# Kernel optimization log

Hardware: AMD Instinct MI355X
Metric: run time of the kernel (lower is better)

Reference implementation:

```python
import jax, jax.numpy as jnp
import numpy as np
import math

C = 512          # channels
K = 3            # conv kernel size
DILATIONS = (1, 3, 5)
RATIO = 2        # up/down sample ratio
FK = 12          # FIR anti-alias kernel size


def kaiser_sinc_filter1d(cutoff, half_width, kernel_size):
    # BigVGAN alias-free kaiser-windowed sinc lowpass filter
    half_size = kernel_size // 2
    delta_f = 4.0 * half_width
    A = 2.285 * (half_size - 1) * math.pi * delta_f + 7.95
    if A > 50.0:
        beta = 0.1102 * (A - 8.7)
    elif A >= 21.0:
        beta = 0.5842 * (A - 21.0) ** 0.4 + 0.07886 * (A - 21.0)
    else:
        beta = 0.0
    window = np.kaiser(kernel_size, beta)
    if kernel_size % 2 == 0:
        time = np.arange(-half_size, half_size) + 0.5
    else:
        time = np.arange(kernel_size) - half_size
    filt = 2.0 * cutoff * window * np.sinc(2.0 * cutoff * time)
    filt = filt / filt.sum()
    return jnp.asarray(filt, dtype=jnp.float32)

# Up/Down both use cutoff=0.5/ratio, half_width=0.6/ratio, kernel=12
AA_FILTER = kaiser_sinc_filter1d(0.5 / RATIO, 0.6 / RATIO, FK)

UP_PAD = FK // RATIO - 1                               # 5 (replicate pad before transpose conv)
UP_PAD_LEFT = UP_PAD * RATIO + (FK - RATIO) // 2       # 15
UP_PAD_RIGHT = UP_PAD * RATIO + (FK - RATIO + 1) // 2  # 15
DN_PAD_LEFT = FK // 2 - 1                              # 5 (even kernel)
DN_PAD_RIGHT = FK // 2                                 # 6


def _depthwise_conv(x, filt, stride=1, lhs_dilation=1, padding=(0, 0)):
    c = x.shape[1]
    w = jnp.broadcast_to(filt.reshape(1, 1, -1), (c, 1, filt.shape[0]))
    return jax.lax.conv_general_dilated(
        x, w, window_strides=(stride,), padding=[padding],
        lhs_dilation=(lhs_dilation,), dimension_numbers=('NCH', 'OIH', 'NCH'),
        feature_group_count=c)


def upsample2x(x):
    # replicate pad, depthwise transposed conv (lhs-dilated conv w/ flipped kernel), crop, scale
    x = jnp.pad(x, ((0, 0), (0, 0), (UP_PAD, UP_PAD)), mode='edge')
    y = RATIO * _depthwise_conv(x, AA_FILTER[::-1], lhs_dilation=RATIO,
                                padding=(FK - 1, FK - 1))
    return y[..., UP_PAD_LEFT:-UP_PAD_RIGHT]


def downsample2x(x):
    x = jnp.pad(x, ((0, 0), (0, 0), (DN_PAD_LEFT, DN_PAD_RIGHT)), mode='edge')
    return _depthwise_conv(x, AA_FILTER, stride=RATIO)


def snake_log(x, alpha, beta):
    # use_log_scale=True: alpha/beta are exponentiated; x + 1/(b+1e-5) * sin(a*x)^2
    a = jnp.exp(alpha)[None, :, None]
    b = jnp.exp(beta)[None, :, None]
    return x + (1.0 / (b + 1e-5)) * jnp.square(jnp.sin(x * a))


def aliasing_activation(x, alpha, beta):
    return downsample2x(snake_log(upsample2x(x), alpha, beta))


def weight_norm_conv1d(x, v, g, bias, dilation):
    # torch weight_norm dim=0: W[o] = g[o] * v[o] / ||v[o]||
    norm = jnp.sqrt(jnp.sum(v * v, axis=(1, 2), keepdims=True))
    w = g[:, None, None] * v / norm
    pad = (K * dilation - dilation) // 2
    y = jax.lax.conv_general_dilated(
        x, w, window_strides=(1,), padding=[(pad, pad)],
        rhs_dilation=(dilation,), dimension_numbers=('NCH', 'OIH', 'NCH'))
    return y + bias[None, :, None]


def setup_inputs() -> dict:
    key = jax.random.key(0)
    ks = jax.random.split(key, 12)
    B, T = 16, 4096
    return {
        'x': jax.random.normal(ks[0], (B, C, T), dtype=jnp.float32),
        'float_masks': jnp.ones((B, 1, T), dtype=jnp.float32),
        'in_snake_alpha': 0.1 * jax.random.normal(ks[1], (3, C), dtype=jnp.float32),
        'in_snake_beta': 0.1 * jax.random.normal(ks[2], (3, C), dtype=jnp.float32),
        'out_snake_alpha': 0.1 * jax.random.normal(ks[3], (3, C), dtype=jnp.float32),
        'out_snake_beta': 0.1 * jax.random.normal(ks[4], (3, C), dtype=jnp.float32),
        'in_conv_v': 0.05 * jax.random.normal(ks[5], (3, C, C, K), dtype=jnp.float32),
        'in_conv_g': 1.0 + 0.01 * jax.random.normal(ks[6], (3, C), dtype=jnp.float32),
        'in_conv_b': 0.01 * jax.random.normal(ks[7], (3, C), dtype=jnp.float32),
        'out_conv_v': 0.05 * jax.random.normal(ks[8], (3, C, C, K), dtype=jnp.float32),
        'out_conv_g': 1.0 + 0.01 * jax.random.normal(ks[9], (3, C), dtype=jnp.float32),
        'out_conv_b': 0.01 * jax.random.normal(ks[10], (3, C), dtype=jnp.float32),
    }


def reference(x, float_masks, in_snake_alpha, in_snake_beta, out_snake_alpha,
              out_snake_beta, in_conv_v, in_conv_g, in_conv_b, out_conv_v,
              out_conv_g, out_conv_b):
    for i, dilation in enumerate(DILATIONS):
        residuals = x
        x = aliasing_activation(x, in_snake_alpha[i], in_snake_beta[i]) * float_masks
        x = weight_norm_conv1d(x, in_conv_v[i], in_conv_g[i], in_conv_b[i], dilation)
        x = aliasing_activation(x, out_snake_alpha[i], out_snake_beta[i]) * float_masks
        x = weight_norm_conv1d(x, out_conv_v[i], out_conv_g[i], out_conv_b[i], 1)
        x = x + residuals
    return x * float_masks
```

## Files before the change

### kernel.cpp

```cpp
#include <hip/hip_runtime.h>
#include <cmath>

#define BN_ 16
#define CN_ 512
#define TN_ 4096
#define TPAD_ 4112
#define PADR_ 8

typedef float f32x4 __attribute__((ext_vector_type(4)));
typedef __bf16 bf16x8 __attribute__((ext_vector_type(8)));
typedef unsigned short u16x8 __attribute__((ext_vector_type(8)));

struct AAFilt { float g0[6]; float g1[6]; float fE[6]; float fO[6]; };

__device__ __forceinline__ unsigned short f2bf(float f) {
  unsigned u = __builtin_bit_cast(unsigned, f);
  u = (u + 0x7fffu + ((u >> 16) & 1u)) >> 16;
  return (unsigned short)u;
}
__device__ __forceinline__ float bf2f(unsigned short h) {
  return __builtin_bit_cast(float, (unsigned)h << 16);
}

__device__ __forceinline__ void gld16(const void* g, void* l) {
  __builtin_amdgcn_global_load_lds((const __attribute__((address_space(1))) void*)g,
                                   (__attribute__((address_space(3))) void*)l,
                                   16, 0, 0);
}

__global__ __launch_bounds__(256) void prep_w(
    const float* __restrict__ vin, const float* __restrict__ gin,
    const float* __restrict__ vout, const float* __restrict__ gout,
    unsigned short* __restrict__ wpack)
{
  const int o = blockIdx.x;
  const int l = blockIdx.y;
  const int i = l >> 1, oc = l & 1;
  const float* v = (oc ? vout : vin) + (size_t)i * CN_ * CN_ * 3 + (size_t)o * CN_ * 3;
  const float g = (oc ? gout : gin)[i * CN_ + o];
  const int tid = threadIdx.x;

  float a = 0.f;
  for (int j = tid; j < 1536; j += 256) { float x = v[j]; a += x * x; }
  #pragma unroll
  for (int off = 32; off > 0; off >>= 1) a += __shfl_down(a, off);
  __shared__ float red[4];
  if ((tid & 63) == 0) red[tid >> 6] = a;
  __syncthreads();
  const float tot = red[0] + red[1] + red[2] + red[3];
  const float scale = g / sqrtf(tot);
  unsigned short* wl = wpack + (size_t)l * 3 * CN_ * CN_;
  for (int j = tid; j < 1536; j += 256) {
    int c = j / 3, k = j - 3 * c;
    wl[((size_t)k * CN_ + o) * CN_ + c] = f2bf(v[j] * scale);
  }
}

__global__ __launch_bounds__(256) void transpose_in(
    const float* __restrict__ src, unsigned short* __restrict__ dst)
{
  __shared__ float tile[32][33];
  const int b = blockIdx.z, c0 = blockIdx.y * 32, t0 = blockIdx.x * 32;
  const int tx = threadIdx.x & 31, ty = threadIdx.x >> 5;
  const float* s = src + ((size_t)b * CN_ + c0) * TN_ + t0;
  #pragma unroll
  for (int j = 0; j < 32; j += 8) tile[ty + j][tx] = s[(size_t)(ty + j) * TN_ + tx];
  __syncthreads();
  unsigned short* d = dst + ((size_t)b * TN_ + t0) * CN_ + c0;
  #pragma unroll
  for (int j = 0; j < 32; j += 8) d[(size_t)(ty + j) * CN_ + tx] = f2bf(tile[tx][ty + j]);
}

__global__ __launch_bounds__(512) void act_kernel(
    const unsigned short* __restrict__ src, unsigned short* __restrict__ dst,
    const float* __restrict__ alpha, const float* __restrict__ beta,
    const float* __restrict__ mask, AAFilt F)
{
  const int c = threadIdx.x;
  const int b = blockIdx.y;
  const int seg = blockIdx.x;
  const int t0 = seg << 7;
  const float av = expf(alpha[c]);
  const float ib = 1.0f / (expf(beta[c]) + 1e-5f);
  const unsigned short* row = src + (size_t)b * TN_ * CN_ + c;
  unsigned short* drow = dst + (size_t)b * TPAD_ * CN_ + c;
  const float* mrow = mask + (size_t)b * TN_;

  if (seg == 0)  { for (int p = 0; p < PADR_; ++p) drow[(size_t)p * CN_] = 0; }
  if (seg == 31) { for (int p = 0; p < PADR_; ++p) drow[(size_t)(TPAD_ - PADR_ + p) * CN_] = 0; }

  auto ldx = [&](int t) -> float {
    t = t < 0 ? 0 : (t > TN_ - 1 ? TN_ - 1 : t);
    return bf2f(row[(size_t)t * CN_]);
  };

  float xw[6];
  #pragma unroll
  for (int j = 0; j < 6; ++j) xw[j] = ldx(t0 - 5 + j);
  float sE[6], sO[6];
  #pragma unroll
  for (int j = 0; j < 6; ++j) { sE[j] = 0.f; sO[j] = 0.f; }
  float s_last = 0.f;

  auto step = [&](int tau, bool emit) {
    float uO = 0.f, uE = 0.f;
    #pragma unroll
    for (int j = 0; j < 6; ++j) { uO += F.g1[j] * xw[j]; uE += F.g0[j] * xw[j]; }
    float so = __sinf(uO * av); float sOn = uO + ib * so * so;
    float se = __sinf(uE * av); float sEn = uE + ib * se * se;
    if (tau + 2 == TN_ - 1) s_last = sOn;
    if (tau + 2 >= TN_) sOn = s_last;
    if (tau + 3 >= TN_) sEn = s_last;
    #pragma unroll
    for (int j = 0; j < 5; ++j) { sE[j] = sE[j + 1]; sO[j] = sO[j + 1]; }
    sE[5] = sEn; sO[5] = sOn;
    if (emit) {
      float d = 0.f;
      #pragma unroll
      for (int j = 0; j < 6; ++j) d += F.fE[j] * sE[j] + F.fO[j] * sO[j];
      d *= mrow[tau];
      drow[(size_t)(PADR_ + tau) * CN_] = f2bf(d);
    }
    #pragma unroll
    for (int j = 0; j < 5; ++j) xw[j] = xw[j + 1];
    xw[5] = ldx(tau + 6);
  };

  for (int w = 0; w < 5; ++w) step(t0 - 5 + w, false);
  if (t0 == 0) {
    float s0 = sE[3];
    sE[1] = s0; sE[2] = s0;
    sO[1] = s0; sO[2] = s0; sO[3] = s0;
  }
  for (int t = t0; t < t0 + 128; ++t) step(t, true);
}

#define ASZ (144 * 32)
#define BSZ (3 * 128 * 32)

#define VMCNT(n) asm volatile("s_waitcnt vmcnt(" #n ")" ::: "memory")
#define BAR __builtin_amdgcn_s_barrier()
#define PRIO1 __builtin_amdgcn_s_setprio(1)
#define PRIO0 __builtin_amdgcn_s_setprio(0)

#define READ_A4(k) do { \
    _Pragma("unroll") \
    for (int mi_ = 0; mi_ < 4; ++mi_) { \
      const int r_ = rbase[k] + mi_ * 16; \
      const int q_ = q4 ^ ((r_ >> 1) & 3); \
      af[mi_] = __builtin_bit_cast(bf16x8, \
          *(const u16x8*)(A + ((size_t)r_ * 4 + q_) * 8)); \
    } \
  } while (0)

#define READ_B4(k) do { \
    _Pragma("unroll") \
    for (int ni_ = 0; ni_ < 4; ++ni_) { \
      const int ob_ = wn * 64 + ni_ * 16 + l15; \
      const int q_ = q4 ^ ((ob_ >> 1) & 3); \
      bfr[ni_] = __builtin_bit_cast(bf16x8, \
          *(const u16x8*)(Bc + (((size_t)(k) * 128 + ob_) * 4 + q_) * 8)); \
    } \
  } while (0)

#define MFMA16 do { \
    _Pragma("unroll") \
    for (int mi_ = 0; mi_ < 4; ++mi_) { \
      _Pragma("unroll") \
      for (int ni_ = 0; ni_ < 4; ++ni_) \
        acc[mi_][ni_] = __builtin_amdgcn_mfma_f32_16x16x32_bf16( \
            af[mi_], bfr[ni_], acc[mi_][ni_], 0, 0, 0); \
    } \
  } while (0)

template <int MODE, int DIL>
__global__ __launch_bounds__(256, 2) void conv_kernel(
    const unsigned short* __restrict__ act,
    const unsigned short* __restrict__ wp,
    const float* __restrict__ bias,
    const unsigned short* __restrict__ res,
    const float* __restrict__ mask,
    void* __restrict__ outp)
{
  __shared__ __align__(16) unsigned short lA[2 * ASZ];
  __shared__ __align__(16) unsigned short lB[2 * BSZ];

  const int tid = threadIdx.x;
  const int bid = blockIdx.x;
  const int xcd = bid & 7, j = bid >> 3;
  const int ob = j & 3, tile = j >> 2;
  const int tt = tile * 8 + xcd;
  const int b = tt >> 5;
  const int t0 = (tt & 31) << 7;
  const int o0 = ob << 7;

  const int lane = tid & 63;
  const int wave = tid >> 6;
  const int wm = wave >> 1, wn = wave & 1;
  const int l15 = lane & 15, q4 = lane >> 4;

  const f32x4 zero = {0.f, 0.f, 0.f, 0.f};
  f32x4 acc[4][4];
  #pragma unroll
  for (int a = 0; a < 4; ++a)
    #pragma unroll
    for (int n = 0; n < 4; ++n) acc[a][n] = zero;

  const unsigned short* aBase = act + ((size_t)b * TPAD_ + t0) * CN_;

  int rbase[3];
  #pragma unroll
  for (int k = 0; k < 3; ++k) rbase[k] = wm * 64 + l15 + PADR_ + (k - 1) * DIL;

  auto stageA = [&](unsigned short* Ad, int c0) {
    { int p = tid;       int r = p >> 2, pq = p & 3, gq = pq ^ ((r >> 1) & 3);
      gld16(aBase + (size_t)r * CN_ + c0 + gq * 8, Ad + (size_t)p * 8); }
    { int p = tid + 256; int r = p >> 2, pq = p & 3, gq = pq ^ ((r >> 1) & 3);
      gld16(aBase + (size_t)r * CN_ + c0 + gq * 8, Ad + (size_t)p * 8); }
    if (tid < 64) {
      int p = tid + 512;
      int r = p >> 2, pq = p & 3, gq = pq ^ ((r >> 1) & 3);
      gld16(aBase + (size_t)r * CN_ + c0 + gq * 8, Ad + (size_t)p * 8); }
  };
  auto stageB = [&](unsigned short* Bd, int c0, int k) {
    { int p = tid;       int ol = p >> 2, pq = p & 3, gq = pq ^ ((ol >> 1) & 3);
      gld16(wp + ((size_t)(k * CN_) + o0 + ol) * CN_ + c0 + gq * 8,
            Bd + ((size_t)k * 512 + p) * 8); }
    { int p = tid + 256; int ol = p >> 2, pq = p & 3, gq = pq ^ ((ol >> 1) & 3);
      gld16(wp + ((size_t)(k * CN_) + o0 + ol) * CN_ + c0 + gq * 8,
            Bd + ((size_t)k * 512 + p) * 8); }
  };

  stageA(lA, 0); stageB(lB, 0, 0); stageB(lB, 0, 1); stageB(lB, 0, 2);
  VMCNT(4);
  BAR;

  for (int cb = 0; cb < 15; ++cb) {
    const unsigned short* A  = lA + (size_t)(cb & 1) * ASZ;
    const unsigned short* Bc = lB + (size_t)(cb & 1) * BSZ;
    unsigned short* An = lA + (size_t)((cb & 1) ^ 1) * ASZ;
    unsigned short* Bn = lB + (size_t)((cb & 1) ^ 1) * BSZ;
    const int c0n = (cb + 1) * 32;
    bf16x8 af[4], bfr[4];
    READ_A4(0); READ_B4(0); stageA(An, c0n); stageB(Bn, c0n, 0);
    BAR; PRIO1; MFMA16; PRIO0; VMCNT(6); BAR;
    READ_A4(1); READ_B4(1); stageB(Bn, c0n, 1);
    BAR; PRIO1; MFMA16; PRIO0; VMCNT(4); BAR;
    READ_A4(2); READ_B4(2); stageB(Bn, c0n, 2);
    BAR; PRIO1; MFMA16; PRIO0; VMCNT(4); BAR;
  }
  {
    const unsigned short* A  = lA + ASZ;
    const unsigned short* Bc = lB + BSZ;
    bf16x8 af[4], bfr[4];
    READ_A4(0); READ_B4(0);
    BAR; PRIO1; MFMA16; PRIO0; VMCNT(2); BAR;
    READ_A4(1); READ_B4(1);
    BAR; PRIO1; MFMA16; PRIO0; VMCNT(0); BAR;
    READ_A4(2); READ_B4(2);
    BAR; PRIO1; MFMA16; PRIO0;
  }

  const int obase = o0 + wn * 64 + l15;
  const int tbase = t0 + wm * 64 + q4 * 4;

  if (MODE == 0) {
    unsigned short* O = (unsigned short*)outp + (size_t)b * TN_ * CN_;
    #pragma unroll
    for (int ni = 0; ni < 4; ++ni) {
      float bv = bias[obase + ni * 16];
      #pragma unroll
      for (int mi = 0; mi < 4; ++mi) {
        #pragma unroll
        for (int r = 0; r < 4; ++r) {
          int t = tbase + mi * 16 + r;
          O[(size_t)t * CN_ + obase + ni * 16] = f2bf(acc[mi][ni][r] + bv);
        }
      }
    }
  } else if (MODE == 1) {
    unsigned short* O = (unsigned short*)outp + (size_t)b * TN_ * CN_;
    const unsigned short* R = res + (size_t)b * TN_ * CN_;
    #pragma unroll
    for (int ni = 0; ni < 4; ++ni) {
      float bv = bias[obase + ni * 16];
      #pragma unroll
      for (int mi = 0; mi < 4; ++mi) {
        #pragma unroll
        for (int r = 0; r < 4; ++r) {
          int t = tbase + mi * 16 + r;
          size_t ix = (size_t)t * CN_ + obase + ni * 16;
          O[ix] = f2bf(acc[mi][ni][r] + bv + bf2f(R[ix]));
        }
      }
    }
  } else {
    float* O = (float*)outp + (size_t)b * CN_ * TN_;
    const unsigned short* R = res + (size_t)b * TN_ * CN_;
    const float* M = mask + (size_t)b * TN_;
    float bv[4];
    #pragma unroll
    for (int ni = 0; ni < 4; ++ni) bv[ni] = bias[obase + ni * 16];
    #pragma unroll
    for (int mi = 0; mi < 4; ++mi) {
      int t = tbase + mi * 16;
      f32x4 mv = *reinterpret_cast<const f32x4*>(M + t);
      #pragma unroll
      for (int ni = 0; ni < 4; ++ni) {
        f32x4 v;
        #pragma unroll
        for (int r = 0; r < 4; ++r)
          v[r] = (acc[mi][ni][r] + bv[ni] + bf2f(R[(size_t)(t + r) * CN_ + obase + ni * 16])) * mv[r];
        *reinterpret_cast<f32x4*>(O + (size_t)(obase + ni * 16) * TN_ + t) = v;
      }
    }
  }
}

static double bi0(double x) {
  double s = 1.0, t = 1.0, q = x * x * 0.25;
  for (int k = 1; k < 50; ++k) { t *= q / ((double)k * (double)k); s += t; if (t < 1e-18 * s) break; }
  return s;
}
static void make_filt(AAFilt* F) {
  const double PI = 3.14159265358979323846;
  double A = 2.285 * 5.0 * PI * 1.2 + 7.95;
  double beta;
  if (A > 50.0) beta = 0.1102 * (A - 8.7);
  else if (A >= 21.0) beta = 0.5842 * pow(A - 21.0, 0.4) + 0.07886 * (A - 21.0);
  else beta = 0.0;
  double i0b = bi0(beta);
  double f[12], sum = 0.0;
  for (int n = 0; n < 12; ++n) {
    double xx = 2.0 * n / 11.0 - 1.0;
    double w = bi0(beta * sqrt(fmax(0.0, 1.0 - xx * xx))) / i0b;
    double tt = (double)(n - 6) + 0.5;
    double arg = 0.5 * tt;
    double snc = sin(PI * arg) / (PI * arg);
    f[n] = 0.5 * w * snc;
    sum += f[n];
  }
  for (int n = 0; n < 12; ++n) f[n] /= sum;
  for (int j = 0; j < 6; ++j) {
    F->g0[j] = (float)(2.0 * f[11 - 2 * j]);
    F->g1[j] = (float)(2.0 * f[10 - 2 * j]);
    F->fE[j] = (float)f[2 * j + 1];
    F->fO[j] = (float)f[2 * j];
  }
}

extern "C" void kernel_launch(void* const* d_in, const int* in_sizes, int n_in,
                              void* d_out, int out_size, void* d_ws, size_t ws_size,
                              hipStream_t stream)
{
  (void)in_sizes; (void)n_in; (void)out_size; (void)ws_size;
  const float* x    = (const float*)d_in[0];
  const float* mask = (const float*)d_in[1];
  const float* inA  = (const float*)d_in[2];
  const float* inB  = (const float*)d_in[3];
  const float* outA = (const float*)d_in[4];
  const float* outB = (const float*)d_in[5];
  const float* vin  = (const float*)d_in[6];
  const float* gin  = (const float*)d_in[7];
  const float* bin  = (const float*)d_in[8];
  const float* vout = (const float*)d_in[9];
  const float* gout = (const float*)d_in[10];
  const float* bout = (const float*)d_in[11];

  char* ws = (char*)d_ws;
  unsigned short* xta  = (unsigned short*)ws;
  unsigned short* xtb  = (unsigned short*)(ws + 67108864);
  unsigned short* actb = (unsigned short*)(ws + 134217728);
  unsigned short* y1   = (unsigned short*)(ws + 134217728 + 67371008);
  unsigned short* wpk  = (unsigned short*)(ws + 134217728 + 67371008 + 67108864);

  AAFilt F; make_filt(&F);

  prep_w<<<dim3(512, 6), dim3(256), 0, stream>>>(vin, gin, vout, gout, wpk);
  transpose_in<<<dim3(128, 16, 16), dim3(256), 0, stream>>>(x, xta);

  act_kernel<<<dim3(32, 16), dim3(512), 0, stream>>>(
      xta, actb, inA + 0 * CN_, inB + 0 * CN_, mask, F);
  conv_kernel<0, 1><<<dim3(2048), dim3(256), 0, stream>>>(
      actb, wpk + (size_t)0 * 3 * CN_ * CN_, bin + 0 * CN_, nullptr, mask, (void*)y1);
  act_kernel<<<dim3(32, 16), dim3(512), 0, stream>>>(
      y1, actb, outA + 0 * CN_, outB + 0 * CN_, mask, F);
  conv_kernel<1, 1><<<dim3(2048), dim3(256), 0, stream>>>(
      actb, wpk + (size_t)1 * 3 * CN_ * CN_, bout + 0 * CN_, xta, mask, (void*)xtb);

  act_kernel<<<dim3(32, 16), dim3(512), 0, stream>>>(
      xtb, actb, inA + 1 * CN_, inB + 1 * CN_, mask, F);
  conv_kernel<0, 3><<<dim3(2048), dim3(256), 0, stream>>>(
      actb, wpk + (size_t)2 * 3 * CN_ * CN_, bin + 1 * CN_, nullptr, mask, (void*)y1);
  act_kernel<<<dim3(32, 16), dim3(512), 0, stream>>>(
      y1, actb, outA + 1 * CN_, outB + 1 * CN_, mask, F);
  conv_kernel<1, 1><<<dim3(2048), dim3(256), 0, stream>>>(
      actb, wpk + (size_t)3 * 3 * CN_ * CN_, bout + 1 * CN_, xtb, mask, (void*)xta);

  act_kernel<<<dim3(32, 16), dim3(512), 0, stream>>>(
      xta, actb, inA + 2 * CN_, inB + 2 * CN_, mask, F);
  conv_kernel<0, 5><<<dim3(2048), dim3(256), 0, stream>>>(
      actb, wpk + (size_t)4 * 3 * CN_ * CN_, bin + 2 * CN_, nullptr, mask, (void*)y1);
  act_kernel<<<dim3(32, 16), dim3(512), 0, stream>>>(
      y1, actb, outA + 2 * CN_, outB + 2 * CN_, mask, F);
  conv_kernel<2, 1><<<dim3(2048), dim3(256), 0, stream>>>(
      actb, wpk + (size_t)5 * 3 * CN_ * CN_, bout + 2 * CN_, xta, mask, d_out);
}
```

Baseline: 1.109 ms.

## Use four-slot ring buffer for weight tiles to raise occupancy to three blocks

Replaces the double-buffered 3-tap weight LDS area (6 slots) with a 4-slot rotating ring indexed by a running tap counter. This shrinks shared memory per block so launch bounds can request 3 blocks per CU instead of 2, hiding latency through more resident waves. The trade is a tighter pipeline: only one tap of lookahead for weight loads, changed vmcnt waits, and a lower register budget under the higher occupancy bound, which may cause spills.

```diff
diff --git a/kernel.cpp b/kernel.cpp
--- a/kernel.cpp
+++ b/kernel.cpp
@@ -136,7 +136,7 @@
 }
 
 #define ASZ (144 * 32)
-#define BSZ (3 * 128 * 32)
+#define BSLOT (128 * 32)
 
 #define VMCNT(n) asm volatile("s_waitcnt vmcnt(" #n ")" ::: "memory")
 #define BAR __builtin_amdgcn_s_barrier()
@@ -153,13 +153,14 @@
     } \
   } while (0)
 
-#define READ_B4(k) do { \
+#define READ_B4(slot) do { \
+    const unsigned short* Bs_ = lB + (size_t)(slot) * BSLOT; \
     _Pragma("unroll") \
     for (int ni_ = 0; ni_ < 4; ++ni_) { \
       const int ob_ = wn * 64 + ni_ * 16 + l15; \
       const int q_ = q4 ^ ((ob_ >> 1) & 3); \
       bfr[ni_] = __builtin_bit_cast(bf16x8, \
-          *(const u16x8*)(Bc + (((size_t)(k) * 128 + ob_) * 4 + q_) * 8)); \
+          *(const u16x8*)(Bs_ + ((size_t)ob_ * 4 + q_) * 8)); \
     } \
   } while (0)
 
@@ -174,7 +175,7 @@
   } while (0)
 
 template <int MODE, int DIL>
-__global__ __launch_bounds__(256, 2) void conv_kernel(
+__global__ __launch_bounds__(256, 3) void conv_kernel(
     const unsigned short* __restrict__ act,
     const unsigned short* __restrict__ wp,
     const float* __restrict__ bias,
@@ -183,7 +184,7 @@
     void* __restrict__ outp)
 {
   __shared__ __align__(16) unsigned short lA[2 * ASZ];
-  __shared__ __align__(16) unsigned short lB[2 * BSZ];
+  __shared__ __align__(16) unsigned short lB[4 * BSLOT];
 
   const int tid = threadIdx.x;
   const int bid = blockIdx.x;
@@ -222,42 +223,46 @@
       int r = p >> 2, pq = p & 3, gq = pq ^ ((r >> 1) & 3);
       gld16(aBase + (size_t)r * CN_ + c0 + gq * 8, Ad + (size_t)p * 8); }
   };
-  auto stageB = [&](unsigned short* Bd, int c0, int k) {
+  auto stageB = [&](int slot, int c0, int k) {
+    unsigned short* Bd = lB + (size_t)slot * BSLOT;
     { int p = tid;       int ol = p >> 2, pq = p & 3, gq = pq ^ ((ol >> 1) & 3);
       gld16(wp + ((size_t)(k * CN_) + o0 + ol) * CN_ + c0 + gq * 8,
-            Bd + ((size_t)k * 512 + p) * 8); }
+            Bd + (size_t)p * 8); }
     { int p = tid + 256; int ol = p >> 2, pq = p & 3, gq = pq ^ ((ol >> 1) & 3);
       gld16(wp + ((size_t)(k * CN_) + o0 + ol) * CN_ + c0 + gq * 8,
-            Bd + ((size_t)k * 512 + p) * 8); }
+            Bd + (size_t)p * 8); }
   };
 
-  stageA(lA, 0); stageB(lB, 0, 0); stageB(lB, 0, 1); stageB(lB, 0, 2);
+  stageA(lA, 0);
+  stageB(0, 0, 0); stageB(1, 0, 1); stageB(2, 0, 2);
   VMCNT(4);
   BAR;
 
   for (int cb = 0; cb < 15; ++cb) {
-    const unsigned short* A  = lA + (size_t)(cb & 1) * ASZ;
-    const unsigned short* Bc = lB + (size_t)(cb & 1) * BSZ;
+    const unsigned short* A = lA + (size_t)(cb & 1) * ASZ;
     unsigned short* An = lA + (size_t)((cb & 1) ^ 1) * ASZ;
-    unsigned short* Bn = lB + (size_t)((cb & 1) ^ 1) * BSZ;
     const int c0n = (cb + 1) * 32;
+    const int tau = 3 * cb;
     bf16x8 af[4], bfr[4];
-    READ_A4(0); READ_B4(0); stageA(An, c0n); stageB(Bn, c0n, 0);
+    READ_A4(0); READ_B4(tau & 3);
+    stageA(An, c0n); stageB((tau + 3) & 3, c0n, 0);
     BAR; PRIO1; MFMA16; PRIO0; VMCNT(6); BAR;
-    READ_A4(1); READ_B4(1); stageB(Bn, c0n, 1);
+    READ_A4(1); READ_B4((tau + 1) & 3);
+    stageB((tau + 4) & 3, c0n, 1);
+    BAR; PRIO1; MFMA16; PRIO0; VMCNT(6); BAR;
+    READ_A4(2); READ_B4((tau + 2) & 3);
+    stageB((tau + 5) & 3, c0n, 2);
     BAR; PRIO1; MFMA16; PRIO0; VMCNT(4); BAR;
-    READ_A4(2); READ_B4(2); stageB(Bn, c0n, 2);
-    BAR; PRIO1; MFMA16; PRIO0; VMCNT(4); BAR;
   }
   {
-    const unsigned short* A  = lA + ASZ;
-    const unsigned short* Bc = lB + BSZ;
+    const unsigned short* A = lA + ASZ;
+    const int tau = 45;
     bf16x8 af[4], bfr[4];
-    READ_A4(0); READ_B4(0);
+    READ_A4(0); READ_B4(tau & 3);
     BAR; PRIO1; MFMA16; PRIO0; VMCNT(2); BAR;
-    READ_A4(1); READ_B4(1);
+    READ_A4(1); READ_B4((tau + 1) & 3);
     BAR; PRIO1; MFMA16; PRIO0; VMCNT(0); BAR;
-    READ_A4(2); READ_B4(2);
+    READ_A4(2); READ_B4((tau + 2) & 3);
     BAR; PRIO1; MFMA16; PRIO0;
   }
 
```

Measured after the change: 1.095 ms, median of 2. Within noise of the previous version (-1.3%).
